# Kernel tuning notes

Hardware: AMD Instinct MI355X
Metric: run time of the kernel (lower is better)

## Reference

```python
import jax, jax.numpy as jnp
import numpy as np

N = 8192          # number of nodes
DIN = 512         # in_features
DOUT = 256        # out_features
P_EDGE = 0.004    # ~32 avg degree
NEG_INF = -9e15   # matches the torch module's -9000000000000000.0 mask value


def setup_inputs() -> dict:
    key = jax.random.key(0)
    ks = jax.random.split(key, 7)
    x = jax.random.normal(ks[0], (N, DIN), dtype=jnp.float32)
    # binary adjacency, Bernoulli(P_EDGE)
    adj = (jax.random.uniform(ks[1], (N, N)) < P_EDGE).astype(jnp.float32)
    W1 = jax.random.normal(ks[2], (DIN, DOUT), dtype=jnp.float32) * 0.05
    b1 = jnp.zeros((DOUT,), dtype=jnp.float32)
    a1_w = jax.random.normal(ks[3], (DOUT,), dtype=jnp.float32) * 0.05
    a1_b = jnp.zeros((), dtype=jnp.float32)
    a2_w = jax.random.normal(ks[4], (DOUT,), dtype=jnp.float32) * 0.05
    a2_b = jnp.zeros((), dtype=jnp.float32)
    return {"x": x, "adj": adj, "W1": W1, "b1": b1,
            "a1_w": a1_w, "a1_b": a1_b, "a2_w": a2_w, "a2_b": a2_b}


def reference(x, adj, W1, b1, a1_w, a1_b, a2_w, a2_b):
    # h = linear1(elu(x))                       [n, DOUT]
    h = jnp.matmul(jax.nn.elu(x), W1) + b1
    # per-node scalar scores g1 (source/col) and g2 (dest/row)
    g1 = h @ a1_w + a1_b                       # [n]
    g2 = h @ a2_w + a2_b                       # [n]
    # kron trick collapses to: scores[i,j] = adj[i,j] * (g2[i] + g1[j])
    scores = adj * (g2[:, None] + g1[None, :])  # [n, n]
    e = jax.nn.leaky_relu(scores, negative_slope=0.2)
    attention = jax.nn.softmax(jnp.where(adj > 0, e, NEG_INF), axis=1)
    # untied=False path: weighted aggregation of h (dropout p=0 is identity)
    return attention @ h
```

## Files before the change

kernel.cpp:

```cpp
#include <hip/hip_runtime.h>
#include <hip/hip_bf16.h>
#include <cstdint>
#include <cstddef>

#define N_NODES 8192
#define DIN 512
#define DOUT 256
#define CAP 128

typedef short bf16x8 __attribute__((ext_vector_type(8)));
typedef float f32x4 __attribute__((ext_vector_type(4)));
typedef unsigned int u32x4 __attribute__((ext_vector_type(4)));

__device__ __forceinline__ float bf2f(unsigned short u) {
    union { unsigned int ui; float f; } v; v.ui = ((unsigned int)u) << 16; return v.f;
}
__device__ __forceinline__ unsigned short f2bf(float f) {
    union { float f; unsigned int u; } v; v.f = f;
    unsigned int u = v.u;
    return (unsigned short)((u + 0x7fffu + ((u >> 16) & 1u)) >> 16);
}
__device__ __forceinline__ float elu1(float v) { return v > 0.f ? v : (expf(v) - 1.f); }

__global__ __launch_bounds__(256) void convw_kernel(
    const float* __restrict__ W1, unsigned short* __restrict__ wb)
{
    const int n = blockIdx.x;
    const int k = threadIdx.x * 2;
    unsigned short a = f2bf(W1[(size_t)k * DOUT + n]);
    unsigned short b = f2bf(W1[(size_t)(k + 1) * DOUT + n]);
    *(unsigned int*)(wb + (size_t)n * DIN + k) = (unsigned int)a | ((unsigned int)b << 16);
}

__global__ __launch_bounds__(256) void gemm_h_kernel(
    const float* __restrict__ x, const unsigned short* __restrict__ wb,
    const float* __restrict__ b1,
    const float* __restrict__ a1w, const float* __restrict__ a1b,
    const float* __restrict__ a2w, const float* __restrict__ a2b,
    unsigned short* __restrict__ h, float* __restrict__ g1, float* __restrict__ g2)
{
    const int tid = threadIdx.x;
    const int wave = tid >> 6, lane = tid & 63;
    const int quad = lane >> 4, r16 = lane & 15;
    const int m0 = blockIdx.x * 16;
    const int n0 = wave * 64;

    f32x4 acc[4] = {{0.f,0.f,0.f,0.f},{0.f,0.f,0.f,0.f},{0.f,0.f,0.f,0.f},{0.f,0.f,0.f,0.f}};
    const float* xrow = x + (size_t)(m0 + r16) * DIN;

    for (int k0 = 0; k0 < DIN; k0 += 32) {
        const int kb = k0 + quad * 8;
        float4 f0 = *(const float4*)(xrow + kb);
        float4 f1 = *(const float4*)(xrow + kb + 4);
        bf16x8 A;
        A[0] = (short)f2bf(elu1(f0.x)); A[1] = (short)f2bf(elu1(f0.y));
        A[2] = (short)f2bf(elu1(f0.z)); A[3] = (short)f2bf(elu1(f0.w));
        A[4] = (short)f2bf(elu1(f1.x)); A[5] = (short)f2bf(elu1(f1.y));
        A[6] = (short)f2bf(elu1(f1.z)); A[7] = (short)f2bf(elu1(f1.w));
        bf16x8 B[4];
        #pragma unroll
        for (int s = 0; s < 4; ++s)
            B[s] = *(const bf16x8*)(wb + (size_t)(n0 + s * 16 + r16) * DIN + kb);
        #pragma unroll
        for (int ni = 0; ni < 4; ++ni)
            acc[ni] = __builtin_amdgcn_mfma_f32_16x16x32_bf16(A, B[ni], acc[ni], 0, 0, 0);
    }

    float p1[4] = {0.f, 0.f, 0.f, 0.f};
    float p2[4] = {0.f, 0.f, 0.f, 0.f};
    #pragma unroll
    for (int ni = 0; ni < 4; ++ni) {
        const int col = n0 + ni * 16 + r16;
        const float bias = b1[col];
        const float w1c = a1w[col], w2c = a2w[col];
        #pragma unroll
        for (int rr = 0; rr < 4; ++rr) {
            float val = acc[ni][rr] + bias;
            h[(size_t)(m0 + quad * 4 + rr) * DOUT + col] = f2bf(val);
            p1[rr] += val * w1c;
            p2[rr] += val * w2c;
        }
    }
    #pragma unroll
    for (int off = 1; off < 16; off <<= 1) {
        #pragma unroll
        for (int rr = 0; rr < 4; ++rr) {
            p1[rr] += __shfl_xor(p1[rr], off, 64);
            p2[rr] += __shfl_xor(p2[rr], off, 64);
        }
    }
    __shared__ float sg1[16][4];
    __shared__ float sg2[16][4];
    if (r16 == 0) {
        #pragma unroll
        for (int rr = 0; rr < 4; ++rr) {
            sg1[quad * 4 + rr][wave] = p1[rr];
            sg2[quad * 4 + rr][wave] = p2[rr];
        }
    }
    __syncthreads();
    if (tid < 16) {
        float t1 = sg1[tid][0] + sg1[tid][1] + sg1[tid][2] + sg1[tid][3];
        float t2 = sg2[tid][0] + sg2[tid][1] + sg2[tid][2] + sg2[tid][3];
        g1[m0 + tid] = t1 + a1b[0];
        g2[m0 + tid] = t2 + a2b[0];
    }
}

__global__ __launch_bounds__(256) void agg_kernel(
    const float* __restrict__ adj, const unsigned short* __restrict__ h,
    const float* __restrict__ g1, const float* __restrict__ g2,
    float* __restrict__ out)
{
    __shared__ int   eidx[4][CAP];
    __shared__ float ev[4][CAP];
    __shared__ int   wcnt[4];

    const int tid  = threadIdx.x;
    const int w    = tid >> 6;
    const int lane = tid & 63;
    const int i    = blockIdx.x * 4 + w;

    if (lane == 0) wcnt[w] = 0;

    const float g2i = g2[i];
    const float* arow = adj + (size_t)i * N_NODES;

    #pragma unroll 1
    for (int g = 0; g < 4; ++g) {
        u32x4 raws[8];
        #pragma unroll
        for (int c = 0; c < 8; ++c)
            raws[c] = __builtin_nontemporal_load(
                (const u32x4*)(arow + (g * 8 + c) * 256 + lane * 4));
        #pragma unroll
        for (int c = 0; c < 8; ++c) {
            u32x4 raw = raws[c];
            if (raw.x | raw.y | raw.z | raw.w) {
                unsigned int wv[4] = {raw.x, raw.y, raw.z, raw.w};
                #pragma unroll
                for (int q = 0; q < 4; ++q) {
                    if (wv[q]) {
                        int j = (g * 8 + c) * 256 + lane * 4 + q;
                        float s = g2i + g1[j];
                        float lr = s > 0.f ? s : 0.2f * s;
                        int pos = atomicAdd(&wcnt[w], 1);
                        if (pos < CAP) { eidx[w][pos] = j; ev[w][pos] = lr; }
                    }
                }
            }
        }
    }

    int K = wcnt[w];
    if (K > CAP) K = CAP;

    if (K == 0) {
        f32x4 acc = {0.f, 0.f, 0.f, 0.f};
        for (int j = 0; j < N_NODES; ++j) {
            ushort4 hv = *(const ushort4*)(h + (size_t)j * DOUT + lane * 4);
            acc[0] += bf2f(hv.x); acc[1] += bf2f(hv.y);
            acc[2] += bf2f(hv.z); acc[3] += bf2f(hv.w);
        }
        const float sc = 1.f / (float)N_NODES;
        float4 o = {acc[0] * sc, acc[1] * sc, acc[2] * sc, acc[3] * sc};
        *(float4*)(out + (size_t)i * DOUT + lane * 4) = o;
        return;
    }

    float m = -1e30f;
    for (int k = lane; k < K; k += 64) m = fmaxf(m, ev[w][k]);
    #pragma unroll
    for (int off = 32; off > 0; off >>= 1) m = fmaxf(m, __shfl_xor(m, off, 64));

    float ssum = 0.f;
    for (int k = lane; k < K; k += 64) {
        float p = expf(ev[w][k] - m);
        ev[w][k] = p;
        ssum += p;
    }
    #pragma unroll
    for (int off = 32; off > 0; off >>= 1) ssum += __shfl_xor(ssum, off, 64);
    const float inv = 1.f / ssum;

    const unsigned short* hp = h + lane * 4;
    f32x4 accA = {0.f, 0.f, 0.f, 0.f};
    f32x4 accB = {0.f, 0.f, 0.f, 0.f};
    int k = 0;
    for (; k + 4 <= K; k += 4) {
        float p0 = ev[w][k],     p1 = ev[w][k + 1], p2 = ev[w][k + 2], p3 = ev[w][k + 3];
        int   j0 = eidx[w][k],   j1 = eidx[w][k+1], j2 = eidx[w][k+2], j3 = eidx[w][k+3];
        ushort4 h0 = *(const ushort4*)(hp + (size_t)j0 * DOUT);
        ushort4 h1 = *(const ushort4*)(hp + (size_t)j1 * DOUT);
        ushort4 h2 = *(const ushort4*)(hp + (size_t)j2 * DOUT);
        ushort4 h3 = *(const ushort4*)(hp + (size_t)j3 * DOUT);
        accA[0] += p0 * bf2f(h0.x); accA[1] += p0 * bf2f(h0.y);
        accA[2] += p0 * bf2f(h0.z); accA[3] += p0 * bf2f(h0.w);
        accB[0] += p1 * bf2f(h1.x); accB[1] += p1 * bf2f(h1.y);
        accB[2] += p1 * bf2f(h1.z); accB[3] += p1 * bf2f(h1.w);
        accA[0] += p2 * bf2f(h2.x); accA[1] += p2 * bf2f(h2.y);
        accA[2] += p2 * bf2f(h2.z); accA[3] += p2 * bf2f(h2.w);
        accB[0] += p3 * bf2f(h3.x); accB[1] += p3 * bf2f(h3.y);
        accB[2] += p3 * bf2f(h3.z); accB[3] += p3 * bf2f(h3.w);
    }
    for (; k < K; ++k) {
        float p = ev[w][k];
        ushort4 hv = *(const ushort4*)(hp + (size_t)eidx[w][k] * DOUT);
        accA[0] += p * bf2f(hv.x); accA[1] += p * bf2f(hv.y);
        accA[2] += p * bf2f(hv.z); accA[3] += p * bf2f(hv.w);
    }
    float4 o = {(accA[0] + accB[0]) * inv, (accA[1] + accB[1]) * inv,
                (accA[2] + accB[2]) * inv, (accA[3] + accB[3]) * inv};
    *(float4*)(out + (size_t)i * DOUT + lane * 4) = o;
}

extern "C" void kernel_launch(void* const* d_in, const int* in_sizes, int n_in,
                              void* d_out, int out_size, void* d_ws, size_t ws_size,
                              hipStream_t stream) {
    const float* x   = (const float*)d_in[0];
    const float* adj = (const float*)d_in[1];
    const float* W1  = (const float*)d_in[2];
    const float* b1  = (const float*)d_in[3];
    const float* a1w = (const float*)d_in[4];
    const float* a1b = (const float*)d_in[5];
    const float* a2w = (const float*)d_in[6];
    const float* a2b = (const float*)d_in[7];

    char* w = (char*)d_ws;
    float* g1 = (float*)w;                     w += (size_t)N_NODES * 4;
    float* g2 = (float*)w;                     w += (size_t)N_NODES * 4;
    unsigned short* h  = (unsigned short*)w;   w += (size_t)N_NODES * DOUT * 2;
    unsigned short* wb = (unsigned short*)w;
    float* out = (float*)d_out;

    hipLaunchKernelGGL(convw_kernel,  dim3(256),  dim3(256), 0, stream, W1, wb);
    hipLaunchKernelGGL(gemm_h_kernel, dim3(512),  dim3(256), 0, stream,
                       x, wb, b1, a1w, a1b, a2w, a2b, h, g1, g2);
    hipLaunchKernelGGL(agg_kernel,    dim3(2048), dim3(256), 0, stream, adj, h, g1, g2, out);
}
```

Before: 394.7 us.

## Overlap adjacency scan with GEMM and build edge lists in global memory

```diff
diff --git a/kernel.cpp b/kernel.cpp
--- a/kernel.cpp
+++ b/kernel.cpp
@@ -7,6 +7,8 @@
 #define DIN 512
 #define DOUT 256
 #define CAP 128
+#define GEMM_BLKS 512
+#define SCAN_BLKS 2048
 
 typedef short bf16x8 __attribute__((ext_vector_type(8)));
 typedef float f32x4 __attribute__((ext_vector_type(4)));
@@ -23,137 +25,144 @@
 __device__ __forceinline__ float elu1(float v) { return v > 0.f ? v : (expf(v) - 1.f); }
 
 __global__ __launch_bounds__(256) void convw_kernel(
-    const float* __restrict__ W1, unsigned short* __restrict__ wb)
+    const float* __restrict__ W1, unsigned short* __restrict__ wb, int* __restrict__ ecnt)
 {
     const int n = blockIdx.x;
     const int k = threadIdx.x * 2;
     unsigned short a = f2bf(W1[(size_t)k * DOUT + n]);
     unsigned short b = f2bf(W1[(size_t)(k + 1) * DOUT + n]);
     *(unsigned int*)(wb + (size_t)n * DIN + k) = (unsigned int)a | ((unsigned int)b << 16);
-}
-
-__global__ __launch_bounds__(256) void gemm_h_kernel(
+    if (blockIdx.x < 32) ecnt[blockIdx.x * 256 + threadIdx.x] = 0;
+}
+
+__global__ __launch_bounds__(256) void fused_kernel(
     const float* __restrict__ x, const unsigned short* __restrict__ wb,
     const float* __restrict__ b1,
     const float* __restrict__ a1w, const float* __restrict__ a1b,
     const float* __restrict__ a2w, const float* __restrict__ a2b,
-    unsigned short* __restrict__ h, float* __restrict__ g1, float* __restrict__ g2)
+    unsigned short* __restrict__ h, float* __restrict__ g1, float* __restrict__ g2,
+    const float* __restrict__ adj, int* __restrict__ ecnt, int* __restrict__ ecols)
 {
     const int tid = threadIdx.x;
-    const int wave = tid >> 6, lane = tid & 63;
-    const int quad = lane >> 4, r16 = lane & 15;
-    const int m0 = blockIdx.x * 16;
-    const int n0 = wave * 64;
-
-    f32x4 acc[4] = {{0.f,0.f,0.f,0.f},{0.f,0.f,0.f,0.f},{0.f,0.f,0.f,0.f},{0.f,0.f,0.f,0.f}};
-    const float* xrow = x + (size_t)(m0 + r16) * DIN;
-
-    for (int k0 = 0; k0 < DIN; k0 += 32) {
-        const int kb = k0 + quad * 8;
-        float4 f0 = *(const float4*)(xrow + kb);
-        float4 f1 = *(const float4*)(xrow + kb + 4);
-        bf16x8 A;
-        A[0] = (short)f2bf(elu1(f0.x)); A[1] = (short)f2bf(elu1(f0.y));
-        A[2] = (short)f2bf(elu1(f0.z)); A[3] = (short)f2bf(elu1(f0.w));
-        A[4] = (short)f2bf(elu1(f1.x)); A[5] = (short)f2bf(elu1(f1.y));
-        A[6] = (short)f2bf(elu1(f1.z)); A[7] = (short)f2bf(elu1(f1.w));
-        bf16x8 B[4];
-        #pragma unroll
-        for (int s = 0; s < 4; ++s)
-            B[s] = *(const bf16x8*)(wb + (size_t)(n0 + s * 16 + r16) * DIN + kb);
-        #pragma unroll
-        for (int ni = 0; ni < 4; ++ni)
-            acc[ni] = __builtin_amdgcn_mfma_f32_16x16x32_bf16(A, B[ni], acc[ni], 0, 0, 0);
-    }
-
-    float p1[4] = {0.f, 0.f, 0.f, 0.f};
-    float p2[4] = {0.f, 0.f, 0.f, 0.f};
-    #pragma unroll
-    for (int ni = 0; ni < 4; ++ni) {
-        const int col = n0 + ni * 16 + r16;
-        const float bias = b1[col];
-        const float w1c = a1w[col], w2c = a2w[col];
-        #pragma unroll
-        for (int rr = 0; rr < 4; ++rr) {
-            float val = acc[ni][rr] + bias;
-            h[(size_t)(m0 + quad * 4 + rr) * DOUT + col] = f2bf(val);
-            p1[rr] += val * w1c;
-            p2[rr] += val * w2c;
-        }
-    }
-    #pragma unroll
-    for (int off = 1; off < 16; off <<= 1) {
-        #pragma unroll
-        for (int rr = 0; rr < 4; ++rr) {
-            p1[rr] += __shfl_xor(p1[rr], off, 64);
-            p2[rr] += __shfl_xor(p2[rr], off, 64);
-        }
-    }
-    __shared__ float sg1[16][4];
-    __shared__ float sg2[16][4];
-    if (r16 == 0) {
-        #pragma unroll
-        for (int rr = 0; rr < 4; ++rr) {
-            sg1[quad * 4 + rr][wave] = p1[rr];
-            sg2[quad * 4 + rr][wave] = p2[rr];
-        }
-    }
-    __syncthreads();
-    if (tid < 16) {
-        float t1 = sg1[tid][0] + sg1[tid][1] + sg1[tid][2] + sg1[tid][3];
-        float t2 = sg2[tid][0] + sg2[tid][1] + sg2[tid][2] + sg2[tid][3];
-        g1[m0 + tid] = t1 + a1b[0];
-        g2[m0 + tid] = t2 + a2b[0];
-    }
-}
-
-__global__ __launch_bounds__(256) void agg_kernel(
-    const float* __restrict__ adj, const unsigned short* __restrict__ h,
+
+    if (blockIdx.x < GEMM_BLKS) {
+        const int wave = tid >> 6, lane = tid & 63;
+        const int quad = lane >> 4, r16 = lane & 15;
+        const int m0 = blockIdx.x * 16;
+        const int n0 = wave * 64;
+
+        f32x4 acc[4] = {{0.f,0.f,0.f,0.f},{0.f,0.f,0.f,0.f},{0.f,0.f,0.f,0.f},{0.f,0.f,0.f,0.f}};
+        const float* xrow = x + (size_t)(m0 + r16) * DIN;
+
+        for (int k0 = 0; k0 < DIN; k0 += 32) {
+            const int kb = k0 + quad * 8;
+            float4 f0 = *(const float4*)(xrow + kb);
+            float4 f1 = *(const float4*)(xrow + kb + 4);
+            bf16x8 A;
+            A[0] = (short)f2bf(elu1(f0.x)); A[1] = (short)f2bf(elu1(f0.y));
+            A[2] = (short)f2bf(elu1(f0.z)); A[3] = (short)f2bf(elu1(f0.w));
+            A[4] = (short)f2bf(elu1(f1.x)); A[5] = (short)f2bf(elu1(f1.y));
+            A[6] = (short)f2bf(elu1(f1.z)); A[7] = (short)f2bf(elu1(f1.w));
+            bf16x8 B[4];
+            #pragma unroll
+            for (int s = 0; s < 4; ++s)
+                B[s] = *(const bf16x8*)(wb + (size_t)(n0 + s * 16 + r16) * DIN + kb);
+            #pragma unroll
+            for (int ni = 0; ni < 4; ++ni)
+                acc[ni] = __builtin_amdgcn_mfma_f32_16x16x32_bf16(A, B[ni], acc[ni], 0, 0, 0);
+        }
+
+        float p1[4] = {0.f, 0.f, 0.f, 0.f};
+        float p2[4] = {0.f, 0.f, 0.f, 0.f};
+        #pragma unroll
+        for (int ni = 0; ni < 4; ++ni) {
+            const int col = n0 + ni * 16 + r16;
+            const float bias = b1[col];
+            const float w1c = a1w[col], w2c = a2w[col];
+            #pragma unroll
+            for (int rr = 0; rr < 4; ++rr) {
+                float val = acc[ni][rr] + bias;
+                h[(size_t)(m0 + quad * 4 + rr) * DOUT + col] = f2bf(val);
+                p1[rr] += val * w1c;
+                p2[rr] += val * w2c;
+            }
+        }
+        #pragma unroll
+        for (int off = 1; off < 16; off <<= 1) {
+            #pragma unroll
+            for (int rr = 0; rr < 4; ++rr) {
+                p1[rr] += __shfl_xor(p1[rr], off, 64);
+                p2[rr] += __shfl_xor(p2[rr], off, 64);
+            }
+        }
+        __shared__ float sg1[16][4];
+        __shared__ float sg2[16][4];
+        if (r16 == 0) {
+            #pragma unroll
+            for (int rr = 0; rr < 4; ++rr) {
+                sg1[quad * 4 + rr][wave] = p1[rr];
+                sg2[quad * 4 + rr][wave] = p2[rr];
+            }
+        }
+        __syncthreads();
+        if (tid < 16) {
+            float t1 = sg1[tid][0] + sg1[tid][1] + sg1[tid][2] + sg1[tid][3];
+            float t2 = sg2[tid][0] + sg2[tid][1] + sg2[tid][2] + sg2[tid][3];
+            g1[m0 + tid] = t1 + a1b[0];
+            g2[m0 + tid] = t2 + a2b[0];
+        }
+        return;
+    }
+
+    const int b = blockIdx.x - GEMM_BLKS;
+    const u32x4* a4 = (const u32x4*)adj;
+    const int base = b * 256 + tid;
+    const int stride = SCAN_BLKS * 256;
+
+    #pragma unroll 1
+    for (int g = 0; g < 4; ++g) {
+        u32x4 raws[8];
+        #pragma unroll
+        for (int c = 0; c < 8; ++c)
+            raws[c] = __builtin_nontemporal_load(a4 + (size_t)base + (size_t)(g * 8 + c) * stride);
+        #pragma unroll
+        for (int c = 0; c < 8; ++c) {
+            u32x4 raw = raws[c];
+            if (raw.x | raw.y | raw.z | raw.w) {
+                unsigned int wv[4] = {raw.x, raw.y, raw.z, raw.w};
+                const int fbase = (base + (g * 8 + c) * stride) * 4;
+                #pragma unroll
+                for (int q = 0; q < 4; ++q) {
+                    if (wv[q]) {
+                        int idx = fbase + q;
+                        int i   = idx >> 13;
+                        int col = idx & 8191;
+                        int pos = atomicAdd(&ecnt[i], 1);
+                        if (pos < CAP) ecols[(size_t)i * CAP + pos] = col;
+                    }
+                }
+            }
+        }
+    }
+}
+
+__global__ __launch_bounds__(256) void agg2_kernel(
+    const int* __restrict__ ecnt, const int* __restrict__ ecols,
+    const unsigned short* __restrict__ h,
     const float* __restrict__ g1, const float* __restrict__ g2,
     float* __restrict__ out)
 {
-    __shared__ int   eidx[4][CAP];
-    __shared__ float ev[4][CAP];
-    __shared__ int   wcnt[4];
+    __shared__ float evs[4][CAP];
+    __shared__ int   jls[4][CAP];
 
     const int tid  = threadIdx.x;
     const int w    = tid >> 6;
     const int lane = tid & 63;
     const int i    = blockIdx.x * 4 + w;
 
-    if (lane == 0) wcnt[w] = 0;
-
+    int K = ecnt[i];
+    if (K > CAP) K = CAP;
     const float g2i = g2[i];
-    const float* arow = adj + (size_t)i * N_NODES;
-
-    #pragma unroll 1
-    for (int g = 0; g < 4; ++g) {
-        u32x4 raws[8];
-        #pragma unroll
-        for (int c = 0; c < 8; ++c)
-            raws[c] = __builtin_nontemporal_load(
-                (const u32x4*)(arow + (g * 8 + c) * 256 + lane * 4));
-        #pragma unroll
-        for (int c = 0; c < 8; ++c) {
-            u32x4 raw = raws[c];
-            if (raw.x | raw.y | raw.z | raw.w) {
-                unsigned int wv[4] = {raw.x, raw.y, raw.z, raw.w};
-                #pragma unroll
-                for (int q = 0; q < 4; ++q) {
-                    if (wv[q]) {
-                        int j = (g * 8 + c) * 256 + lane * 4 + q;
-                        float s = g2i + g1[j];
-                        float lr = s > 0.f ? s : 0.2f * s;
-                        int pos = atomicAdd(&wcnt[w], 1);
-                        if (pos < CAP) { eidx[w][pos] = j; ev[w][pos] = lr; }
-                    }
-                }
-            }
-        }
-    }
-
-    int K = wcnt[w];
-    if (K > CAP) K = CAP;
 
     if (K == 0) {
         f32x4 acc = {0.f, 0.f, 0.f, 0.f};
@@ -168,46 +177,57 @@
         return;
     }
 
-    float m = -1e30f;
-    for (int k = lane; k < K; k += 64) m = fmaxf(m, ev[w][k]);
+    float e0 = -1e30f, e1 = -1e30f;
+    int   j0 = 0,      j1 = 0;
+    if (lane < K) {
+        j0 = ecols[(size_t)i * CAP + lane];
+        float s = g2i + g1[j0];
+        e0 = s > 0.f ? s : 0.2f * s;
+    }
+    if (lane + 64 < K) {
+        j1 = ecols[(size_t)i * CAP + lane + 64];
+        float s = g2i + g1[j1];
+        e1 = s > 0.f ? s : 0.2f * s;
+    }
+    float m = fmaxf(e0, e1);
     #pragma unroll
     for (int off = 32; off > 0; off >>= 1) m = fmaxf(m, __shfl_xor(m, off, 64));
 
-    float ssum = 0.f;
-    for (int k = lane; k < K; k += 64) {
-        float p = expf(ev[w][k] - m);
-        ev[w][k] = p;
-        ssum += p;
-    }
+    float p0 = expf(e0 - m);
+    float p1 = expf(e1 - m);
+    float ssum = p0 + p1;
     #pragma unroll
     for (int off = 32; off > 0; off >>= 1) ssum += __shfl_xor(ssum, off, 64);
     const float inv = 1.f / ssum;
+
+    evs[w][lane] = p0;      jls[w][lane] = j0;
+    evs[w][lane + 64] = p1; jls[w][lane + 64] = j1;
 
     const unsigned short* hp = h + lane * 4;
     f32x4 accA = {0.f, 0.f, 0.f, 0.f};
     f32x4 accB = {0.f, 0.f, 0.f, 0.f};
     int k = 0;
     for (; k + 4 <= K; k += 4) {
-        float p0 = ev[w][k],     p1 = ev[w][k + 1], p2 = ev[w][k + 2], p3 = ev[w][k + 3];
-        int   j0 = eidx[w][k],   j1 = eidx[w][k+1], j2 = eidx[w][k+2], j3 = eidx[w][k+3];
-        ushort4 h0 = *(const ushort4*)(hp + (size_t)j0 * DOUT);
-        ushort4 h1 = *(const ushort4*)(hp + (size_t)j1 * DOUT);
-        ushort4 h2 = *(const ushort4*)(hp + (size_t)j2 * DOUT);
-        ushort4 h3 = *(const ushort4*)(hp + (size_t)j3 * DOUT);
-        accA[0] += p0 * bf2f(h0.x); accA[1] += p0 * bf2f(h0.y);
-        accA[2] += p0 * bf2f(h0.z); accA[3] += p0 * bf2f(h0.w);
-        accB[0] += p1 * bf2f(h1.x); accB[1] += p1 * bf2f(h1.y);
-        accB[2] += p1 * bf2f(h1.z); accB[3] += p1 * bf2f(h1.w);
-        accA[0] += p2 * bf2f(h2.x); accA[1] += p2 * bf2f(h2.y);
-        accA[2] += p2 * bf2f(h2.z); accA[3] += p2 * bf2f(h2.w);
-        accB[0] += p3 * bf2f(h3.x); accB[1] += p3 * bf2f(h3.y);
-        accB[2] += p3 * bf2f(h3.z); accB[3] += p3 * bf2f(h3.w);
+        float q0 = evs[w][k],   q1 = evs[w][k+1], q2 = evs[w][k+2], q3 = evs[w][k+3];
+        int   i0 = jls[w][k],   i1 = jls[w][k+1], i2 = jls[w][k+2], i3 = jls[w][k+3];
+        ushort4 h0 = *(const ushort4*)(hp + (size_t)i0 * DOUT);
+        ushort4 h1 = *(const ushort4*)(hp + (size_t)i1 * DOUT);
+        ushort4 h2 = *(const ushort4*)(hp + (size_t)i2 * DOUT);
+        ushort4 h3 = *(const ushort4*)(hp + (size_t)i3 * DOUT);
+        accA[0] += q0 * bf2f(h0.x); accA[1] += q0 * bf2f(h0.y);
+        accA[2] += q0 * bf2f(h0.z); accA[3] += q0 * bf2f(h0.w);
+        accB[0] += q1 * bf2f(h1.x); accB[1] += q1 * bf2f(h1.y);
+        accB[2] += q1 * bf2f(h1.z); accB[3] += q1 * bf2f(h1.w);
+        accA[0] += q2 * bf2f(h2.x); accA[1] += q2 * bf2f(h2.y);
+        accA[2] += q2 * bf2f(h2.z); accA[3] += q2 * bf2f(h2.w);
+        accB[0] += q3 * bf2f(h3.x); accB[1] += q3 * bf2f(h3.y);
+        accB[2] += q3 * bf2f(h3.z); accB[3] += q3 * bf2f(h3.w);
     }
     for (; k < K; ++k) {
-        float p = ev[w][k];
-        ushort4 hv = *(const ushort4*)(hp + (size_t)eidx[w][k] * DOUT);
-        accA[0] += p * bf2f(hv.x); accA[1] += p * bf2f(hv.y);
-        accA[2] += p * bf2f(hv.z); accA[3] += p * bf2f(hv.w);
+        float q = evs[w][k];
+        ushort4 hv = *(const ushort4*)(hp + (size_t)jls[w][k] * DOUT);
+        accA[0] += q * bf2f(hv.x); accA[1] += q * bf2f(hv.y);
+        accA[2] += q * bf2f(hv.z); accA[3] += q * bf2f(hv.w);
     }
     float4 o = {(accA[0] + accB[0]) * inv, (accA[1] + accB[1]) * inv,
                 (accA[2] + accB[2]) * inv, (accA[3] + accB[3]) * inv};
@@ -230,11 +250,13 @@
     float* g1 = (float*)w;                     w += (size_t)N_NODES * 4;
     float* g2 = (float*)w;                     w += (size_t)N_NODES * 4;
     unsigned short* h  = (unsigned short*)w;   w += (size_t)N_NODES * DOUT * 2;
-    unsigned short* wb = (unsigned short*)w;
+    unsigned short* wb = (unsigned short*)w;   w += (size_t)DOUT * DIN * 2;
+    int* ecnt = (int*)w;                       w += (size_t)N_NODES * 4;
+    int* ecols = (int*)w;
     float* out = (float*)d_out;
 
-    hipLaunchKernelGGL(convw_kernel,  dim3(256),  dim3(256), 0, stream, W1, wb);
-    hipLaunchKernelGGL(gemm_h_kernel, dim3(512),  dim3(256), 0, stream,
-                       x, wb, b1, a1w, a1b, a2w, a2b, h, g1, g2);
-    hipLaunchKernelGGL(agg_kernel,    dim3(2048), dim3(256), 0, stream, adj, h, g1, g2, out);
-}
+    hipLaunchKernelGGL(convw_kernel, dim3(256), dim3(256), 0, stream, W1, wb, ecnt);
+    hipLaunchKernelGGL(fused_kernel, dim3(GEMM_BLKS + SCAN_BLKS), dim3(256), 0, stream,
+                       x, wb, b1, a1w, a1b, a2w, a2b, h, g1, g2, adj, ecnt, ecols);
+    hipLaunchKernelGGL(agg2_kernel, dim3(2048), dim3(256), 0, stream, ecnt, ecols, h, g1, g2, out);
+}
```

Result: slower. 420.0 us (+6.4%).
